# Kernel tuning notes

Hardware: AMD Instinct MI355X
Metric: run time of the kernel (lower is better)

## Reference

```python
import jax, jax.numpy as jnp
import numpy as np

N_EMBD = 2048
N_HEAD = 16
N_KV_HEAD = 4
HEAD_DIM = N_EMBD // N_HEAD
MAX_SEQ_LEN = 2048
EPS = 1e-6
ROPE_THETA = 10000.0


def _build_rope_cache(dim, max_seq_len, theta=ROPE_THETA):
    inv_freq = 1.0 / theta ** (np.arange(0, dim, 2, dtype=np.float32) / dim)
    t = np.arange(max_seq_len, dtype=np.float32)
    freqs = np.outer(t, inv_freq)
    emb = np.concatenate([freqs, freqs], axis=-1)
    return jnp.asarray(np.cos(emb)), jnp.asarray(np.sin(emb))


def _rotate_half(x):
    x1, x2 = jnp.split(x, 2, axis=-1)
    return jnp.concatenate([-x2, x1], axis=-1)


def _rms_norm(x, w, eps=EPS):
    var = jnp.mean(jnp.square(x), axis=-1, keepdims=True)
    return x * jax.lax.rsqrt(var + eps) * w


def setup_inputs() -> dict:
    key = jax.random.key(0)
    ks = jax.random.split(key, 7)
    s = 1.0 / np.sqrt(N_EMBD)
    kv_dim = N_KV_HEAD * HEAD_DIM
    x = jax.random.normal(ks[0], (2, 2048, N_EMBD), dtype=jnp.float32)
    Wq = jax.random.normal(ks[1], (N_EMBD, N_EMBD), dtype=jnp.float32) * s
    Wk = jax.random.normal(ks[2], (kv_dim, N_EMBD), dtype=jnp.float32) * s
    Wv = jax.random.normal(ks[3], (kv_dim, N_EMBD), dtype=jnp.float32) * s
    Wo = jax.random.normal(ks[4], (N_EMBD, N_EMBD), dtype=jnp.float32) * s
    qn_w = jnp.ones((HEAD_DIM,), dtype=jnp.float32)
    kn_w = jnp.ones((HEAD_DIM,), dtype=jnp.float32)
    cos, sin = _build_rope_cache(HEAD_DIM, MAX_SEQ_LEN)
    return {"x": x, "Wq": Wq, "Wk": Wk, "Wv": Wv, "Wo": Wo,
            "qn_w": qn_w, "kn_w": kn_w, "rope_cos": cos, "rope_sin": sin}


def reference(x, Wq, Wk, Wv, Wo, qn_w, kn_w, rope_cos, rope_sin):
    B, T, C = x.shape
    # projections (torch Linear: y = x @ W.T)
    q = jnp.einsum('btc,dc->btd', x, Wq).reshape(B, T, N_HEAD, HEAD_DIM).transpose(0, 2, 1, 3)
    k = jnp.einsum('btc,dc->btd', x, Wk).reshape(B, T, N_KV_HEAD, HEAD_DIM).transpose(0, 2, 1, 3)
    v = jnp.einsum('btc,dc->btd', x, Wv).reshape(B, T, N_KV_HEAD, HEAD_DIM).transpose(0, 2, 1, 3)
    # qk rms-norm
    q = _rms_norm(q, qn_w)
    k = _rms_norm(k, kn_w)
    # rope
    cos = rope_cos[:T][None, None]  # [1,1,T,D]
    sin = rope_sin[:T][None, None]
    q = q * cos + _rotate_half(q) * sin
    k = k * cos + _rotate_half(k) * sin
    # GQA broadcast: group queries over kv heads instead of repeating k/v
    G = N_HEAD // N_KV_HEAD
    qg = q.reshape(B, N_KV_HEAD, G, T, HEAD_DIM)
    scale = 1.0 / jnp.sqrt(jnp.asarray(HEAD_DIM, dtype=q.dtype))
    scores = jnp.einsum('bhgqd,bhkd->bhgqk', qg, k) * scale  # [B,KV,G,T,T]
    causal = jnp.tril(jnp.ones((T, T), dtype=bool))
    scores = jnp.where(causal, scores, jnp.asarray(-jnp.inf, dtype=scores.dtype))
    attn = jax.nn.softmax(scores, axis=-1)
    y = jnp.einsum('bhgqk,bhkd->bhgqd', attn, v)  # [B,KV,G,T,D]
    y = y.reshape(B, N_HEAD, T, HEAD_DIM).transpose(0, 2, 1, 3).reshape(B, T, C)
    return jnp.einsum('btc,dc->btd', y, Wo)
```

## Files before the change

kernel.cpp:

```cpp
#include <hip/hip_runtime.h>
#include <stdint.h>

typedef unsigned short u16;
typedef __attribute__((ext_vector_type(4))) float f32x4;
typedef __attribute__((ext_vector_type(16))) float f32x16;
typedef __attribute__((ext_vector_type(8))) short bf16x8;
typedef __attribute__((ext_vector_type(4))) unsigned short u16x4;
typedef __attribute__((ext_vector_type(4))) unsigned u32x4;

static __device__ __forceinline__ u16 f2bf(float f) {
  union { float f; unsigned u; } v; v.f = f;
  unsigned r = v.u + 0x7fffu + ((v.u >> 16) & 1u);
  return (u16)(r >> 16);
}
static __device__ __forceinline__ float bf2f(u16 u) {
  union { unsigned u; float f; } v; v.u = ((unsigned)u) << 16;
  return v.f;
}

static __device__ __forceinline__ unsigned cvtpk(float lo, float hi) {
  unsigned r;
  asm("v_cvt_pk_bf16_f32 %0, %1, %2" : "=v"(r) : "v"(lo), "v"(hi));
  return r;
}

static __device__ __forceinline__ void plane32_swap(unsigned& a, unsigned& b) {
  asm volatile("v_permlane32_swap_b32 %0, %1" : "+v"(a), "+v"(b));
}

static __device__ __forceinline__ float exp2_fast(float x) {
  float r;
  asm("v_exp_f32 %0, %1" : "=v"(r) : "v"(x));
  return r;
}

static __device__ __forceinline__ void load_lds16(const void* g, void* l) {
  __builtin_amdgcn_global_load_lds(
      (const __attribute__((address_space(1))) void*)g,
      (__attribute__((address_space(3))) void*)l, 16, 0, 0);
}

__global__ __launch_bounds__(256) void cvt_all(
    const float* __restrict__ x, const float* __restrict__ Wq,
    const float* __restrict__ Wk, const float* __restrict__ Wv,
    const float* __restrict__ Wo, u16* __restrict__ xb,
    u16* __restrict__ wcat, u16* __restrict__ wob) {
  int i = blockIdx.x * 256 + threadIdx.x;
  const int nx = 2097152, nw = 1572864, total = 4718592;
  for (; i < total; i += gridDim.x * 256) {
    const float* src;
    u16* dst;
    if (i < nx) {
      src = x + (size_t)i * 4;
      dst = xb + (size_t)i * 4;
    } else if (i < nx + nw) {
      int k = i - nx;
      int row = k >> 9, c4 = k & 511;
      const float* s;
      if (row < 2048)      s = Wq + (size_t)row * 2048;
      else if (row < 2560) s = Wk + (size_t)(row - 2048) * 2048;
      else                 s = Wv + (size_t)(row - 2560) * 2048;
      src = s + c4 * 4;
      dst = wcat + (size_t)k * 4;
    } else {
      int k = i - nx - nw;
      src = Wo + (size_t)k * 4;
      dst = wob + (size_t)k * 4;
    }
    f32x4 v = *(const f32x4*)src;
    u16x4 o = { f2bf(v[0]), f2bf(v[1]), f2bf(v[2]), f2bf(v[3]) };
    *(u16x4*)dst = o;
  }
}

#define GEMM_CORE(C_STORE)                                                            \
  __shared__ u16 As[128 * 64];                                                        \
  __shared__ u16 Bs[128 * 64];                                                        \
  const int tid = threadIdx.x;                                                        \
  const int lin = blockIdx.x;                                                         \
  const int x = lin & 7, t = lin >> 3;                              \
  const int bm = x * 4 + (t & 3);                                                     \
  const int bn = t >> 2;                                                              \
  const int w = tid >> 6, l = tid & 63;                                               \
  const int wr = w >> 1, wc = w & 1;                                                  \
  const int ql = l & 31, hi = l >> 5;                                                 \
  f32x16 acc[2][2] = {};                                                              \
  const int nk = K >> 6;                                                              \
  for (int kt = 0; kt < nk; ++kt) {                                                   \
    __syncthreads();                                                                  \
    const int ko = kt << 6;                                                           \
    _Pragma("unroll")                                                                 \
    for (int j = 0; j < 4; ++j) {                                                     \
      int idx = j * 256 + tid;                                                        \
      int row = idx >> 3, ch = idx & 7;                                               \
      int col = ko + (((ch ^ (row & 7))) << 3);                                       \
      load_lds16(A + (size_t)(bm * 128 + row) * K + col, As + idx * 8);               \
      load_lds16(B + (size_t)(bn * 128 + row) * K + col, Bs + idx * 8);               \
    }                                                                                 \
    __syncthreads();                                                                  \
    _Pragma("unroll")                                                                 \
    for (int ks = 0; ks < 4; ++ks) {                                                  \
      const int e = ks * 2 + hi;                                                      \
      bf16x8 af[2], bfr[2];                                                           \
      _Pragma("unroll")                                                               \
      for (int ti = 0; ti < 2; ++ti) {                                                \
        const int ra = wr * 64 + ti * 32 + ql;                                        \
        const int rb = wc * 64 + ti * 32 + ql;                                        \
        af[ti]  = *(const bf16x8*)&As[ra * 64 + ((e ^ (ra & 7)) << 3)];               \
        bfr[ti] = *(const bf16x8*)&Bs[rb * 64 + ((e ^ (rb & 7)) << 3)];               \
      }                                                                               \
      _Pragma("unroll")                                                               \
      for (int mi = 0; mi < 2; ++mi)                                                  \
        _Pragma("unroll")                                                             \
        for (int ni = 0; ni < 2; ++ni)                                                \
          acc[mi][ni] = __builtin_amdgcn_mfma_f32_32x32x16_bf16(                      \
              af[mi], bfr[ni], acc[mi][ni], 0, 0, 0);                                 \
    }                                                                                 \
  }                                                                                   \
  _Pragma("unroll")                                                                   \
  for (int mi = 0; mi < 2; ++mi) {                                                    \
    const int rb0 = bm * 128 + wr * 64 + mi * 32;                                     \
    _Pragma("unroll")                                                                 \
    for (int ni = 0; ni < 2; ++ni) {                                                  \
      const int col = bn * 128 + wc * 64 + ni * 32 + ql;                              \
      _Pragma("unroll")                                                               \
      for (int r = 0; r < 16; ++r) {                                                  \
        const int row = rb0 + (r & 3) + 8 * (r >> 2) + 4 * hi;                        \
        C_STORE;                                                                      \
      }                                                                               \
    }                                                                                 \
  }

__global__ __launch_bounds__(256) void gemm_bt16(
    const u16* __restrict__ A, const u16* __restrict__ B,
    u16* __restrict__ C, int M, int N, int K) {
  GEMM_CORE(C[(size_t)row * N + col] = f2bf(acc[mi][ni][r]))
}

__global__ __launch_bounds__(256) void gemm_bt(
    const u16* __restrict__ A, const u16* __restrict__ B,
    float* __restrict__ C, int M, int N, int K) {
  GEMM_CORE(C[(size_t)row * N + col] = acc[mi][ni][r])
}

__global__ __launch_bounds__(256) void norm_rope(
    const u16* __restrict__ qkv, const float* __restrict__ qn_w,
    const float* __restrict__ kn_w, const float* __restrict__ cosb,
    const float* __restrict__ sinb, u16* __restrict__ qhat,
    u16* __restrict__ khat) {
  const int gw = (blockIdx.x * 256 + threadIdx.x) >> 6;
  const int lane = threadIdx.x & 63;
  const int slot = gw % 20;
  const int row = gw / 20;
  const int t = row & 2047;
  const int b = row >> 11;
  const u16* src; const float* nw; u16* dst;
  bool isq = slot < 16;
  if (isq) {
    src = qkv + (size_t)row * 3072 + slot * 128;
    nw = qn_w;
    dst = qhat + ((size_t)(b * 16 + slot) * 2048 + t) * 128;
  } else {
    src = qkv + (size_t)row * 3072 + 2048 + (slot - 16) * 128;
    nw = kn_w;
    dst = khat + ((size_t)(b * 4 + (slot - 16)) * 2048 + t) * 128;
  }
  float x1 = bf2f(src[lane]), x2 = bf2f(src[lane + 64]);
  float ss = x1 * x1 + x2 * x2;
#pragma unroll
  for (int o = 32; o; o >>= 1) ss += __shfl_xor(ss, o);
  float rs = rsqrtf(ss * (1.0f / 128.0f) + 1e-6f);
  float h1 = x1 * rs * nw[lane];
  float h2 = x2 * rs * nw[lane + 64];
  float c = cosb[t * 128 + lane], s = sinb[t * 128 + lane];
  float o1 = h1 * c - h2 * s;
  float o2 = h2 * c + h1 * s;
  if (isq) { o1 *= 0.12751744752f; o2 *= 0.12751744752f; }
  dst[lane] = f2bf(o1);
  dst[lane + 64] = f2bf(o2);
}

__global__ __launch_bounds__(256) void v_trans(
    const u16* __restrict__ qkv, u16* __restrict__ vT) {
  __shared__ u16 st[64][130];
  const int bi = blockIdx.x;
  const int tt = bi & 31;
  const int kv = (bi >> 5) & 3;
  const int b = bi >> 7;
  const int tid = threadIdx.x;
#pragma unroll
  for (int i = 0; i < 32; ++i) {
    int idx = i * 256 + tid;
    int t = idx >> 7, d = idx & 127;
    st[t][d] = qkv[(size_t)(b * 2048 + tt * 64 + t) * 3072 + 2560 + kv * 128 + d];
  }
  __syncthreads();
#pragma unroll
  for (int i = 0; i < 32; ++i) {
    int idx = i * 256 + tid;
    int d = idx >> 6, t = idx & 63;
    vT[((size_t)(b * 4 + kv) * 128 + d) * 2048 + tt * 64 + t] = st[t][d];
  }
}

__global__ __launch_bounds__(256, 2) void attn(
    const u16* __restrict__ qhat, const u16* __restrict__ khat,
    const u16* __restrict__ vT, u16* __restrict__ yb) {
  __shared__ u16 Kt[2][64 * 128];
  __shared__ u16 Vt[2][128 * 64];
  const int bi = blockIdx.x;
  const int j = bi & 255;
  const int pairup = bi >> 8;
  const int bh = j >> 3;
  const int cc = j & 7;
  const int c = pairup ? (15 - cc) : cc;
  const int h = bh & 15, b = bh >> 4;
  const int kvh = h >> 2;
  const int tid = threadIdx.x;
  const int w = tid >> 6, l = tid & 63;
  const int ql = l & 31, hi = l >> 5;
  const int wq0 = c * 128 + w * 32;
  const int wq_end = wq0 + 31;
  const int qg = wq0 + ql;

  bf16x8 qf[8];
  const u16* qp = qhat + ((size_t)(b * 16 + h) * 2048 + qg) * 128 + hi * 8;
#pragma unroll
  for (int sf = 0; sf < 8; ++sf) qf[sf] = *(const bf16x8*)(qp + 16 * sf);

  f32x16 yacc[4] = {};
  float m = -1e30f, lsum = 0.f;

  const u16* Kg = khat + (size_t)(b * 4 + kvh) * 2048 * 128;
  const u16* Vg = vT + (size_t)(b * 4 + kvh) * 128 * 2048;
  const int nt = 2 * c + 2;

  auto stageK = [&](int tile, int buf) {
#pragma unroll
    for (int jj = 0; jj < 4; ++jj) {
      int idx = jj * 256 + tid;
      int row = idx >> 4, ch = idx & 15;
      load_lds16(Kg + (size_t)(tile * 64 + row) * 128 + ((ch ^ (row & 7)) * 8),
                 &Kt[buf][idx * 8]);
    }
  };
  auto stageV = [&](int tile, int buf) {
#pragma unroll
    for (int jj = 0; jj < 4; ++jj) {
      int idx = jj * 256 + tid;
      int row = idx >> 3, ch = idx & 7;
      load_lds16(Vg + (size_t)row * 2048 + tile * 64 + ((ch ^ (row & 7)) * 8),
                 &Vt[buf][idx * 8]);
    }
  };

  stageK(0, 0);
  stageV(0, 0);
  int cur = 0;
  for (int tile = 0; tile < nt; ++tile) {
    const int kv0 = tile * 64;
    __syncthreads();
    if (tile + 1 < nt) { stageK(tile + 1, cur ^ 1); stageV(tile + 1, cur ^ 1); }
    if (kv0 <= wq_end) {
      const u16* Kc = Kt[cur];
      const u16* Vc = Vt[cur];
      f32x16 sacc[2] = {};
      __builtin_amdgcn_s_setprio(1);
#pragma unroll
      for (int n = 0; n < 2; ++n) {
#pragma unroll
        for (int sf = 0; sf < 8; ++sf) {
          bf16x8 kf = *(const bf16x8*)&Kc[(n * 32 + ql) * 128 + (((2 * sf + hi) ^ (l & 7)) * 8)];
          sacc[n] = __builtin_amdgcn_mfma_f32_32x32x16_bf16(kf, qf[sf], sacc[n], 0, 0, 0);
        }
      }
      __builtin_amdgcn_s_setprio(0);
      if (kv0 + 63 > wq0) {
#pragma unroll
        for (int n = 0; n < 2; ++n)
#pragma unroll
          for (int r = 0; r < 16; ++r) {
            int kv = kv0 + n * 32 + (r & 3) + 8 * (r >> 2) + 4 * hi;
            if (kv > qg) sacc[n][r] = -1e30f;
          }
      }
      float pm = -1e30f;
#pragma unroll
      for (int n = 0; n < 2; ++n)
#pragma unroll
        for (int r = 0; r < 16; ++r) pm = fmaxf(pm, sacc[n][r]);
      pm = fmaxf(pm, __shfl_xor(pm, 32));
      if (!__all(pm - m <= 11.0f)) {
        float mn = fmaxf(m, pm);
        float sc = exp2_fast(m - mn);
        m = mn;
        lsum *= sc;
#pragma unroll
        for (int r = 0; r < 16; ++r) {
          int row = (r & 3) + 8 * (r >> 2) + 4 * hi;
          float scr = __shfl(sc, row);
#pragma unroll
          for (int d = 0; d < 4; ++d) yacc[d][r] *= scr;
        }
      }
      float ls = 0.f;
#pragma unroll
      for (int n = 0; n < 2; ++n)
#pragma unroll
        for (int r = 0; r < 16; ++r) {
          float e = exp2_fast(sacc[n][r] - m);
          sacc[n][r] = e;
          ls += e;
        }
      ls += __shfl_xor(ls, 32);
      lsum += ls;
      bf16x8 pa[4];
#pragma unroll
      for (int s4 = 0; s4 < 4; ++s4) {
        const int n = s4 >> 1, R = (s4 & 1) * 8;
        unsigned P01 = cvtpk(sacc[n][R + 0], sacc[n][R + 1]);
        unsigned P23 = cvtpk(sacc[n][R + 2], sacc[n][R + 3]);
        unsigned P45 = cvtpk(sacc[n][R + 4], sacc[n][R + 5]);
        unsigned P67 = cvtpk(sacc[n][R + 6], sacc[n][R + 7]);
        plane32_swap(P01, P45);
        plane32_swap(P23, P67);
        union { u32x4 u; bf16x8 bv; } cvu;
        cvu.u[0] = P01; cvu.u[1] = P23; cvu.u[2] = P45; cvu.u[3] = P67;
        pa[s4] = cvu.bv;
      }
      __builtin_amdgcn_s_setprio(1);
#pragma unroll
      for (int d = 0; d < 4; ++d) {
        const int rv = d * 32 + ql;
#pragma unroll
        for (int ks = 0; ks < 4; ++ks) {
          bf16x8 vf = *(const bf16x8*)&Vc[rv * 64 + (((ks * 2 + hi) ^ (rv & 7)) * 8)];
          yacc[d] = __builtin_amdgcn_mfma_f32_32x32x16_bf16(pa[ks], vf, yacc[d], 0, 0, 0);
        }
      }
      __builtin_amdgcn_s_setprio(0);
    }
    cur ^= 1;
  }
#pragma unroll
  for (int r = 0; r < 16; ++r) {
    int row = (r & 3) + 8 * (r >> 2) + 4 * hi;
    float li = __shfl(lsum, row);
    float inv = 1.0f / li;
    u16* yp = yb + ((size_t)(b * 2048) + wq0 + row) * 2048 + h * 128 + ql;
#pragma unroll
    for (int d = 0; d < 4; ++d) yp[d * 32] = f2bf(yacc[d][r] * inv);
  }
}


extern "C" void kernel_launch(void* const* d_in, const int* in_sizes, int n_in,
                              void* d_out, int out_size, void* d_ws, size_t ws_size,
                              hipStream_t stream) {
  const float* x    = (const float*)d_in[0];
  const float* Wq   = (const float*)d_in[1];
  const float* Wk   = (const float*)d_in[2];
  const float* Wv   = (const float*)d_in[3];
  const float* Wo   = (const float*)d_in[4];
  const float* qn   = (const float*)d_in[5];
  const float* kn   = (const float*)d_in[6];
  const float* cosb = (const float*)d_in[7];
  const float* sinb = (const float*)d_in[8];
  float* out = (float*)d_out;
  (void)in_sizes; (void)n_in; (void)out_size; (void)ws_size;

  char* p = (char*)d_ws;
  u16*   xb   = (u16*)p;   p += (size_t)8388608 * 2;
  u16*   wcat = (u16*)p;   p += (size_t)6291456 * 2;
  u16*   wob  = (u16*)p;   p += (size_t)4194304 * 2;
  u16*   qkvb = (u16*)p;   p += (size_t)12582912 * 2;
  u16*   qh   = (u16*)p;   p += (size_t)8388608 * 2;
  u16*   kh   = (u16*)p;   p += (size_t)2097152 * 2;
  u16*   vt   = (u16*)p;   p += (size_t)2097152 * 2;
  u16*   yb   = (u16*)p;   p += (size_t)8388608 * 2;

  cvt_all<<<2048, 256, 0, stream>>>(x, Wq, Wk, Wv, Wo, xb, wcat, wob);
  gemm_bt16<<<768, 256, 0, stream>>>(xb, wcat, qkvb, 4096, 3072, 2048);
  norm_rope<<<20480, 256, 0, stream>>>(qkvb, qn, kn, cosb, sinb, qh, kh);
  v_trans<<<256, 256, 0, stream>>>(qkvb, vt);
  attn<<<512, 256, 0, stream>>>(qh, kh, vt, yb);
  gemm_bt<<<512, 256, 0, stream>>>(yb, wob, out, 4096, 2048, 2048);
}
```

Baseline: 209.3 us.

## Software-pipeline attention: overlap next tile's QK^T with current softmax and PV

Restructures the attention kernel's KV-tile loop into a two-stage pipeline. The QK^T MFMAs for tile t now run before the softmax and P·V step of tile t-1, using two ping-pong score accumulators (sA/sB) and an unrolled-by-two loop. The V shared-memory buffer grows from two to three slots so tile t-1's V stays valid while later tiles are staged. This is meant to let the matrix units work while the vector units do exp and max. In exchange it raises register pressure from the second score accumulator and uses more LDS.

```diff
diff --git a/kernel.cpp b/kernel.cpp
--- a/kernel.cpp
+++ b/kernel.cpp
@@ -207,7 +207,7 @@
     const u16* __restrict__ qhat, const u16* __restrict__ khat,
     const u16* __restrict__ vT, u16* __restrict__ yb) {
   __shared__ u16 Kt[2][64 * 128];
-  __shared__ u16 Vt[2][128 * 64];
+  __shared__ u16 Vt[3][128 * 64];
   const int bi = blockIdx.x;
   const int j = bi & 255;
   const int pairup = bi >> 8;
@@ -254,94 +254,120 @@
     }
   };
 
+  auto qkt = [&](const u16* Kc, f32x16 (&s)[2]) {
+    __builtin_amdgcn_s_setprio(1);
+#pragma unroll
+    for (int n = 0; n < 2; ++n) {
+#pragma unroll
+      for (int sf = 0; sf < 8; ++sf) {
+        bf16x8 kf = *(const bf16x8*)&Kc[(n * 32 + ql) * 128 + (((2 * sf + hi) ^ (l & 7)) * 8)];
+        s[n] = __builtin_amdgcn_mfma_f32_32x32x16_bf16(kf, qf[sf], s[n], 0, 0, 0);
+      }
+    }
+    __builtin_amdgcn_s_setprio(0);
+  };
+  auto finish = [&](int tp, f32x16 (&s)[2]) {
+    const int kv0 = tp * 64;
+    if (kv0 > wq_end) return;
+    if (kv0 + 63 > wq0) {
+#pragma unroll
+      for (int n = 0; n < 2; ++n)
+#pragma unroll
+        for (int r = 0; r < 16; ++r) {
+          int kv = kv0 + n * 32 + (r & 3) + 8 * (r >> 2) + 4 * hi;
+          if (kv > qg) s[n][r] = -1e30f;
+        }
+    }
+    float pm = -1e30f;
+#pragma unroll
+    for (int n = 0; n < 2; ++n)
+#pragma unroll
+      for (int r = 0; r < 16; ++r) pm = fmaxf(pm, s[n][r]);
+    pm = fmaxf(pm, __shfl_xor(pm, 32));
+    if (!__all(pm - m <= 11.0f)) {
+      float mn = fmaxf(m, pm);
+      float sc = exp2_fast(m - mn);
+      m = mn;
+      lsum *= sc;
+#pragma unroll
+      for (int r = 0; r < 16; ++r) {
+        int row = (r & 3) + 8 * (r >> 2) + 4 * hi;
+        float scr = __shfl(sc, row);
+#pragma unroll
+        for (int d = 0; d < 4; ++d) yacc[d][r] *= scr;
+      }
+    }
+    float ls = 0.f;
+#pragma unroll
+    for (int n = 0; n < 2; ++n)
+#pragma unroll
+      for (int r = 0; r < 16; ++r) {
+        float e = exp2_fast(s[n][r] - m);
+        s[n][r] = e;
+        ls += e;
+      }
+    ls += __shfl_xor(ls, 32);
+    lsum += ls;
+    bf16x8 pa[4];
+#pragma unroll
+    for (int s4 = 0; s4 < 4; ++s4) {
+      const int n = s4 >> 1, R = (s4 & 1) * 8;
+      unsigned P01 = cvtpk(s[n][R + 0], s[n][R + 1]);
+      unsigned P23 = cvtpk(s[n][R + 2], s[n][R + 3]);
+      unsigned P45 = cvtpk(s[n][R + 4], s[n][R + 5]);
+      unsigned P67 = cvtpk(s[n][R + 6], s[n][R + 7]);
+      plane32_swap(P01, P45);
+      plane32_swap(P23, P67);
+      union { u32x4 u; bf16x8 bv; } cvu;
+      cvu.u[0] = P01; cvu.u[1] = P23; cvu.u[2] = P45; cvu.u[3] = P67;
+      pa[s4] = cvu.bv;
+    }
+    const u16* Vc = Vt[tp % 3];
+    __builtin_amdgcn_s_setprio(1);
+#pragma unroll
+    for (int d = 0; d < 4; ++d) {
+      const int rv = d * 32 + ql;
+#pragma unroll
+      for (int ks = 0; ks < 4; ++ks) {
+        bf16x8 vf = *(const bf16x8*)&Vc[rv * 64 + (((ks * 2 + hi) ^ (rv & 7)) * 8)];
+        yacc[d] = __builtin_amdgcn_mfma_f32_32x32x16_bf16(pa[ks], vf, yacc[d], 0, 0, 0);
+      }
+    }
+    __builtin_amdgcn_s_setprio(0);
+  };
+  auto zero2 = [&](f32x16 (&s)[2]) {
+#pragma unroll
+    for (int r = 0; r < 16; ++r) { s[0][r] = 0.f; s[1][r] = 0.f; }
+  };
+
   stageK(0, 0);
   stageV(0, 0);
-  int cur = 0;
-  for (int tile = 0; tile < nt; ++tile) {
-    const int kv0 = tile * 64;
+  __syncthreads();
+  if (nt > 1) { stageK(1, 1); stageV(1, 1); }
+  f32x16 sA[2], sB[2];
+  zero2(sA);
+  qkt(Kt[0], sA);
+
+  int t = 1;
+  for (; t + 1 < nt; t += 2) {
     __syncthreads();
-    if (tile + 1 < nt) { stageK(tile + 1, cur ^ 1); stageV(tile + 1, cur ^ 1); }
-    if (kv0 <= wq_end) {
-      const u16* Kc = Kt[cur];
-      const u16* Vc = Vt[cur];
-      f32x16 sacc[2] = {};
-      __builtin_amdgcn_s_setprio(1);
-#pragma unroll
-      for (int n = 0; n < 2; ++n) {
-#pragma unroll
-        for (int sf = 0; sf < 8; ++sf) {
-          bf16x8 kf = *(const bf16x8*)&Kc[(n * 32 + ql) * 128 + (((2 * sf + hi) ^ (l & 7)) * 8)];
-          sacc[n] = __builtin_amdgcn_mfma_f32_32x32x16_bf16(kf, qf[sf], sacc[n], 0, 0, 0);
-        }
-      }
-      __builtin_amdgcn_s_setprio(0);
-      if (kv0 + 63 > wq0) {
-#pragma unroll
-        for (int n = 0; n < 2; ++n)
-#pragma unroll
-          for (int r = 0; r < 16; ++r) {
-            int kv = kv0 + n * 32 + (r & 3) + 8 * (r >> 2) + 4 * hi;
-            if (kv > qg) sacc[n][r] = -1e30f;
-          }
-      }
-      float pm = -1e30f;
-#pragma unroll
-      for (int n = 0; n < 2; ++n)
-#pragma unroll
-        for (int r = 0; r < 16; ++r) pm = fmaxf(pm, sacc[n][r]);
-      pm = fmaxf(pm, __shfl_xor(pm, 32));
-      if (!__all(pm - m <= 11.0f)) {
-        float mn = fmaxf(m, pm);
-        float sc = exp2_fast(m - mn);
-        m = mn;
-        lsum *= sc;
-#pragma unroll
-        for (int r = 0; r < 16; ++r) {
-          int row = (r & 3) + 8 * (r >> 2) + 4 * hi;
-          float scr = __shfl(sc, row);
-#pragma unroll
-          for (int d = 0; d < 4; ++d) yacc[d][r] *= scr;
-        }
-      }
-      float ls = 0.f;
-#pragma unroll
-      for (int n = 0; n < 2; ++n)
-#pragma unroll
-        for (int r = 0; r < 16; ++r) {
-          float e = exp2_fast(sacc[n][r] - m);
-          sacc[n][r] = e;
-          ls += e;
-        }
-      ls += __shfl_xor(ls, 32);
-      lsum += ls;
-      bf16x8 pa[4];
-#pragma unroll
-      for (int s4 = 0; s4 < 4; ++s4) {
-        const int n = s4 >> 1, R = (s4 & 1) * 8;
-        unsigned P01 = cvtpk(sacc[n][R + 0], sacc[n][R + 1]);
-        unsigned P23 = cvtpk(sacc[n][R + 2], sacc[n][R + 3]);
-        unsigned P45 = cvtpk(sacc[n][R + 4], sacc[n][R + 5]);
-        unsigned P67 = cvtpk(sacc[n][R + 6], sacc[n][R + 7]);
-        plane32_swap(P01, P45);
-        plane32_swap(P23, P67);
-        union { u32x4 u; bf16x8 bv; } cvu;
-        cvu.u[0] = P01; cvu.u[1] = P23; cvu.u[2] = P45; cvu.u[3] = P67;
-        pa[s4] = cvu.bv;
-      }
-      __builtin_amdgcn_s_setprio(1);
-#pragma unroll
-      for (int d = 0; d < 4; ++d) {
-        const int rv = d * 32 + ql;
-#pragma unroll
-        for (int ks = 0; ks < 4; ++ks) {
-          bf16x8 vf = *(const bf16x8*)&Vc[rv * 64 + (((ks * 2 + hi) ^ (rv & 7)) * 8)];
-          yacc[d] = __builtin_amdgcn_mfma_f32_32x32x16_bf16(pa[ks], vf, yacc[d], 0, 0, 0);
-        }
-      }
-      __builtin_amdgcn_s_setprio(0);
-    }
-    cur ^= 1;
-  }
+    stageK(t + 1, (t + 1) & 1);
+    stageV(t + 1, (t + 1) % 3);
+    zero2(sB);
+    if (t * 64 <= wq_end) qkt(Kt[t & 1], sB);
+    finish(t - 1, sA);
+    __syncthreads();
+    if (t + 2 < nt) { stageK(t + 2, (t + 2) & 1); stageV(t + 2, (t + 2) % 3); }
+    zero2(sA);
+    if ((t + 1) * 64 <= wq_end) qkt(Kt[(t + 1) & 1], sA);
+    finish(t, sB);
+  }
+  __syncthreads();
+  zero2(sB);
+  if (t * 64 <= wq_end) qkt(Kt[t & 1], sB);
+  finish(t - 1, sA);
+  finish(t, sB);
+
 #pragma unroll
   for (int r = 0; r < 16; ++r) {
     int row = (r & 3) + 8 * (r >> 2) + 4 * hi;
```

Measured after the change: 211.1 us. Within noise of the previous version (+0.9%).
